# Kernel optimization log

Measured on AMD Instinct MI355X. Metric: run time of the kernel, lower is better.

Reference implementation:

```python
import jax, jax.numpy as jnp
import numpy as np

B, S, D, H = 2, 2048, 1024, 16
DK = D // H

def setup_inputs() -> dict:
    key = jax.random.key(0)
    ks = jax.random.split(key, 11)
    scale = 1.0 / np.sqrt(D)
    inp = {
        'Q': jax.random.normal(ks[0], (B, S, D), jnp.float32),
        'K': jax.random.normal(ks[1], (B, S, D), jnp.float32),
        'V': jax.random.normal(ks[2], (B, S, D), jnp.float32),
        'Wq': jax.random.normal(ks[3], (D, D), jnp.float32) * scale,
        'bq': jax.random.normal(ks[4], (D,), jnp.float32) * 0.01,
        'Wk': jax.random.normal(ks[5], (D, D), jnp.float32) * scale,
        'bk': jax.random.normal(ks[6], (D,), jnp.float32) * 0.01,
        'Wv': jax.random.normal(ks[7], (D, D), jnp.float32) * scale,
        'bv': jax.random.normal(ks[8], (D,), jnp.float32) * 0.01,
        'Wo': jax.random.normal(ks[9], (D, D), jnp.float32) * scale,
        'bo': jax.random.normal(ks[10], (D,), jnp.float32) * 0.01,
    }
    return inp

def reference(Q, K, V, Wq, bq, Wk, bk, Wv, bv, Wo, bo):
    bs = Q.shape[0]
    # projections (torch Linear: x @ W.T + b), reshape to [b, h, s, d_k]
    q = (Q @ Wq.T + bq).reshape(bs, -1, H, DK).transpose(0, 2, 1, 3)
    k = (K @ Wk.T + bk).reshape(bs, -1, H, DK).transpose(0, 2, 1, 3)
    v = (V @ Wv.T + bv).reshape(bs, -1, H, DK).transpose(0, 2, 1, 3)
    # scaled dot-product attention (no mask, dropout p=0)
    scores = jnp.einsum('bhqd,bhkd->bhqk', q, k) / np.sqrt(DK).astype(np.float32)
    attn = jax.nn.softmax(scores, axis=-1)
    ctx = jnp.einsum('bhqk,bhkd->bhqd', attn, v)
    concat = ctx.transpose(0, 2, 1, 3).reshape(bs, -1, D)
    return concat @ Wo.T + bo
```

## Files before the change

### kernel.cpp

```cpp
#include <hip/hip_runtime.h>
#include <hip/hip_bf16.h>
#include <stdint.h>

#define B_  2
#define S_  2048
#define D_  1024
#define H_  16
#define DK_ 64
#define M_  (B_ * S_)

#define QSCALE 0.18033688011112042f

typedef __attribute__((ext_vector_type(4)))  float f32x4;
typedef __attribute__((ext_vector_type(16))) float f32x16;
typedef __attribute__((ext_vector_type(8)))  short bf16x8;

__device__ __forceinline__ unsigned short f2bf(float f) {
    union { float f; unsigned u; } a; a.f = f;
    unsigned u = a.u;
    unsigned r = (u + 0x7fffu + ((u >> 16) & 1u)) >> 16;
    return (unsigned short)r;
}
__device__ __forceinline__ unsigned pk2(float lo, float hi) {
    union { float f; unsigned u; } a, b; a.f = lo; b.f = hi;
    unsigned ra = a.u + 0x7fffu + ((a.u >> 16) & 1u);
    unsigned rb = b.u + 0x7fffu + ((b.u >> 16) & 1u);
    return __builtin_amdgcn_perm(rb, ra, 0x07060302u);
}
__device__ __forceinline__ unsigned pk2f(float lo, float hi) {
    union { float f; unsigned u; } a, b; a.f = lo; b.f = hi;
    return __builtin_amdgcn_perm(b.u + 0x8000u, a.u + 0x8000u, 0x07060302u);
}

__device__ __forceinline__ void gload16(const void* g, void* l) {
    __builtin_amdgcn_global_load_lds(
        (const __attribute__((address_space(1))) void*)g,
        (__attribute__((address_space(3))) void*)l, 16, 0, 0);
}

__global__ __launch_bounds__(256) void cvt_all(
    const float* __restrict__ p0, const float* __restrict__ p1,
    const float* __restrict__ p2, const float* __restrict__ p3,
    const float* __restrict__ p4, const float* __restrict__ p5,
    const float* __restrict__ p6,
    unsigned short* __restrict__ o0, unsigned short* __restrict__ o1,
    unsigned short* __restrict__ o2, unsigned short* __restrict__ o3,
    unsigned short* __restrict__ o4, unsigned short* __restrict__ o5,
    unsigned short* __restrict__ o6) {
    const int y = blockIdx.y;
    if (y >= 3 && blockIdx.x >= 512) return;
    const float* in = (y == 0) ? p0 : (y == 1) ? p1 : (y == 2) ? p2 :
                      (y == 3) ? p3 : (y == 4) ? p4 : (y == 5) ? p5 : p6;
    unsigned short* out = (y == 0) ? o0 : (y == 1) ? o1 : (y == 2) ? o2 :
                          (y == 3) ? o3 : (y == 4) ? o4 : (y == 5) ? o5 : o6;
    const int i = blockIdx.x * 256 + threadIdx.x;
    const float4* p = (const float4*)in + (size_t)i * 2;
    float4 u = p[0], v = p[1];
    union { unsigned us[4]; bf16x8 v; } o;
    o.us[0] = pk2(u.x, u.y); o.us[1] = pk2(u.z, u.w);
    o.us[2] = pk2(v.x, v.y); o.us[3] = pk2(v.z, v.w);
    *((bf16x8*)out + i) = o.v;
}

__device__ __forceinline__ void gemm128_core(const unsigned short* __restrict__ A,
                                             const unsigned short* __restrict__ Bw,
                                             unsigned short* As, unsigned short* Bs,
                                             int brow, int bcol, f32x4 (&acc)[4][4]) {
    constexpr int K = D_;
    const int t = threadIdx.x;
    const int l = t & 63;
    const int l15 = l & 15, l4 = l >> 4;
    const int wr = (t >> 6) >> 1, wc = (t >> 6) & 1;

    const unsigned short* Ap = A + (size_t)(brow + (t >> 2)) * K + (t & 3) * 8;
    const unsigned short* Bp = Bw + (size_t)(bcol + (t >> 2)) * K + (t & 3) * 8;
    unsigned short* AsT = As + t * 8;
    unsigned short* BsT = Bs + t * 8;

    for (int k0 = 0; k0 < K; k0 += 32) {
        __syncthreads();
        gload16(Ap + k0, AsT);
        gload16(Ap + 64 * K + k0, AsT + 2048);
        gload16(Bp + k0, BsT);
        gload16(Bp + 64 * K + k0, BsT + 2048);
        __syncthreads();

        bf16x8 af[4], bfv[4];
#pragma unroll
        for (int m = 0; m < 4; m++)
            af[m] = *(const bf16x8*)(As + (wr * 64 + m * 16 + l15) * 32 + l4 * 8);
#pragma unroll
        for (int n = 0; n < 4; n++)
            bfv[n] = *(const bf16x8*)(Bs + (wc * 64 + n * 16 + l15) * 32 + l4 * 8);
#pragma unroll
        for (int m = 0; m < 4; m++)
#pragma unroll
            for (int n = 0; n < 4; n++)
                acc[m][n] = __builtin_amdgcn_mfma_f32_16x16x32_bf16(af[m], bfv[n],
                                                                    acc[m][n], 0, 0, 0);
    }
}

__global__ __launch_bounds__(256) void gemm_qkv(
    const unsigned short* __restrict__ xq, const unsigned short* __restrict__ xk,
    const unsigned short* __restrict__ xv,
    const unsigned short* __restrict__ wq, const unsigned short* __restrict__ wk,
    const unsigned short* __restrict__ wv,
    const float* __restrict__ bq, const float* __restrict__ bk,
    const float* __restrict__ bv,
    unsigned short* __restrict__ oq, unsigned short* __restrict__ ok,
    unsigned short* __restrict__ ov) {
    __shared__ unsigned short As[128 * 32];
    __shared__ unsigned short Bs[128 * 32];

    const int z = blockIdx.z;
    const unsigned short* A  = (z == 0) ? xq : (z == 1) ? xk : xv;
    const unsigned short* Bw = (z == 0) ? wq : (z == 1) ? wk : wv;
    const float* bias        = (z == 0) ? bq : (z == 1) ? bk : bv;
    unsigned short* out      = (z == 0) ? oq : (z == 1) ? ok : ov;

    const int brow = blockIdx.y * 128;
    const int bcol = blockIdx.x * 128;
    const f32x4 zf = {0.0f, 0.0f, 0.0f, 0.0f};
    f32x4 acc[4][4];
#pragma unroll
    for (int i = 0; i < 4; i++)
#pragma unroll
        for (int j = 0; j < 4; j++) acc[i][j] = zf;

    gemm128_core(A, Bw, As, Bs, brow, bcol, acc);

    const int t = threadIdx.x;
    const int l = t & 63;
    const int l15 = l & 15, l4 = l >> 4;
    const int wr = (t >> 6) >> 1, wc = (t >> 6) & 1;
    const float scale = (z == 0) ? QSCALE : 1.0f;

#pragma unroll
    for (int n = 0; n < 4; n++) {
        const int col = bcol + wc * 64 + n * 16 + l15;
        const float bia = bias[col];
        const int h = col >> 6, dk = col & 63;
#pragma unroll
        for (int m = 0; m < 4; m++) {
            const int row0 = brow + wr * 64 + m * 16 + l4 * 4;
            const int b = row0 >> 11, s0 = row0 & (S_ - 1);
            if (z != 2) {
#pragma unroll
                for (int r = 0; r < 4; r++) {
                    float v = (acc[m][n][r] + bia) * scale;
                    out[((size_t)((b * H_ + h) * S_ + (s0 + r))) * DK_ + dk] = f2bf(v);
                }
            } else {
                const int st = s0 >> 7, sl = s0 & 127;
                const int g16 = (sl >> 2) & 3;
                const int sig = ((g16 & 1) << 1) | (g16 >> 1);
                const int y = (((sl >> 4) << 5) + (sig << 3)) ^ ((dk & 7) << 4);
                uint2 o;
                o.x = pk2(acc[m][n][0] + bia, acc[m][n][1] + bia);
                o.y = pk2(acc[m][n][2] + bia, acc[m][n][3] + bia);
                *(uint2*)((char*)out +
                          ((((size_t)(b * H_ + h) * 16 + st) * 64 + dk) << 8) + y) = o;
            }
        }
    }
}

__global__ __launch_bounds__(256) void gemm_out(const unsigned short* __restrict__ A,
                                                const unsigned short* __restrict__ Bw,
                                                const float* __restrict__ bias,
                                                float* __restrict__ out) {
    __shared__ unsigned short As[128 * 32];
    __shared__ unsigned short Bs[128 * 32];

    const int brow = blockIdx.y * 128;
    const int bcol = blockIdx.x * 128;
    const f32x4 zf = {0.0f, 0.0f, 0.0f, 0.0f};
    f32x4 acc[4][4];
#pragma unroll
    for (int i = 0; i < 4; i++)
#pragma unroll
        for (int j = 0; j < 4; j++) acc[i][j] = zf;

    gemm128_core(A, Bw, As, Bs, brow, bcol, acc);

    const int t = threadIdx.x;
    const int l = t & 63;
    const int l15 = l & 15, l4 = l >> 4;
    const int wr = (t >> 6) >> 1, wc = (t >> 6) & 1;
#pragma unroll
    for (int n = 0; n < 4; n++) {
        const int col = bcol + wc * 64 + n * 16 + l15;
        const float bia = bias[col];
#pragma unroll
        for (int m = 0; m < 4; m++) {
            const int row0 = brow + wr * 64 + m * 16 + l4 * 4;
#pragma unroll
            for (int r = 0; r < 4; r++)
                out[(size_t)(row0 + r) * D_ + col] = acc[m][n][r] + bia;
        }
    }
}

__global__ __launch_bounds__(512, 4) void attn_kernel(const unsigned short* __restrict__ qh,
                                                      const unsigned short* __restrict__ kh,
                                                      const unsigned short* __restrict__ vimg,
                                                      unsigned short* __restrict__ ctx) {
    __shared__ unsigned short smem[2][16384];
    char* sm = (char*)smem;

    const int t = threadIdx.x;
    const int w = t >> 6, l = t & 63;
    const int l31 = l & 31, hi = l >> 5;
    const int hi16 = hi * 16;
    const int swz = (l31 & 7) << 4;
    const int grp = w >> 2;
    const int qs  = w & 3;

    const int bid = blockIdx.x;
    const int bh = (bid & 7) * 4 + ((bid >> 3) & 3);
    const int qt = bid >> 5;
    const int b = bh >> 4, h = bh & 15;

    const unsigned short* qg = qh + (size_t)bh * S_ * DK_;
    const unsigned short* kg = kh + (size_t)bh * S_ * DK_;

    const int q0 = qt * 128 + qs * 32;

    bf16x8 qf[4];
#pragma unroll
    for (int kc = 0; kc < 4; kc++)
        qf[kc] = *(const bf16x8*)(qg + (size_t)(q0 + l31) * DK_ + kc * 16 + hi * 8);

    const f32x16 zf16 = {0.0f};
    f32x16 acc0 = zf16, acc1 = zf16;
    float lpart = 0.0f;

    const int klr = t >> 3;
    const int kchunk = (t & 7) ^ (klr & 7);
    const unsigned short* kgp = kg + (size_t)klr * DK_ + kchunk * 8;
    auto STAGE_K = [&](int j, int buf) {
        const unsigned short* src = kgp + (size_t)j * 128 * DK_;
        char* dst = sm + buf * 32768 + t * 16;
        gload16(src, dst);
        gload16(src + 64 * DK_, dst + 8192);
    };
    const unsigned short* vgp = vimg + (size_t)bh * (16 * 8192) + t * 8;
    auto STAGE_V = [&](int j, int buf) {
        const unsigned short* src = vgp + j * 8192;
        char* dst = sm + buf * 32768 + 16384 + t * 16;
        gload16(src, dst);
        gload16(src + 4096, dst + 8192);
    };

    STAGE_K(0, 0);
    STAGE_V(0, 0);
    __syncthreads();

    constexpr int NT2 = S_ / 128;
    for (int j = 0; j < NT2; ++j) {
        const int cur = j & 1;
        if (j + 1 < NT2) {
            STAGE_K(j + 1, cur ^ 1);
            STAGE_V(j + 1, cur ^ 1);
        }

        const char* Kb = sm + cur * 32768 + grp * 8192;
        const char* Vb = sm + cur * 32768 + 16384 + grp * 128;

        f32x16 st0, st1;
        __builtin_amdgcn_s_setprio(1);
        {
            bf16x8 k0 = *(const bf16x8*)(Kb + l31 * 128 + (hi16 ^ swz));
            bf16x8 k1 = *(const bf16x8*)(Kb + (32 + l31) * 128 + (hi16 ^ swz));
            st0 = __builtin_amdgcn_mfma_f32_32x32x16_bf16(k0, qf[0], zf16, 0, 0, 0);
            st1 = __builtin_amdgcn_mfma_f32_32x32x16_bf16(k1, qf[0], zf16, 0, 0, 0);
        }
#pragma unroll
        for (int kc = 1; kc < 4; kc++) {
            bf16x8 k0 = *(const bf16x8*)(Kb + l31 * 128 + ((kc * 32 + hi16) ^ swz));
            bf16x8 k1 = *(const bf16x8*)(Kb + (32 + l31) * 128 + ((kc * 32 + hi16) ^ swz));
            st0 = __builtin_amdgcn_mfma_f32_32x32x16_bf16(k0, qf[kc], st0, 0, 0, 0);
            st1 = __builtin_amdgcn_mfma_f32_32x32x16_bf16(k1, qf[kc], st1, 0, 0, 0);
        }
        __builtin_amdgcn_s_setprio(0);

#pragma unroll
        for (int i = 0; i < 16; i++) st0[i] = exp2f(st0[i]);
#pragma unroll
        for (int i = 0; i < 16; i++) st1[i] = exp2f(st1[i]);

        float sv[8];
#pragma unroll
        for (int i = 0; i < 8; i++) sv[i] = (st0[i] + st0[i + 8]) + (st1[i] + st1[i + 8]);
#pragma unroll
        for (int s = 4; s >= 1; s >>= 1)
#pragma unroll
            for (int i = 0; i < s; i++) sv[i] += sv[i + s];
        lpart += sv[0];

        bf16x8 pf[4];
        {
            union { unsigned u[4]; bf16x8 v; } pu;
            pu.u[0] = pk2f(st0[0], st0[1]);   pu.u[1] = pk2f(st0[2], st0[3]);
            pu.u[2] = pk2f(st0[4], st0[5]);   pu.u[3] = pk2f(st0[6], st0[7]);
            pf[0] = pu.v;
            pu.u[0] = pk2f(st0[8], st0[9]);   pu.u[1] = pk2f(st0[10], st0[11]);
            pu.u[2] = pk2f(st0[12], st0[13]); pu.u[3] = pk2f(st0[14], st0[15]);
            pf[1] = pu.v;
            pu.u[0] = pk2f(st1[0], st1[1]);   pu.u[1] = pk2f(st1[2], st1[3]);
            pu.u[2] = pk2f(st1[4], st1[5]);   pu.u[3] = pk2f(st1[6], st1[7]);
            pf[2] = pu.v;
            pu.u[0] = pk2f(st1[8], st1[9]);   pu.u[1] = pk2f(st1[10], st1[11]);
            pu.u[2] = pk2f(st1[12], st1[13]); pu.u[3] = pk2f(st1[14], st1[15]);
            pf[3] = pu.v;
        }

        __builtin_amdgcn_s_setprio(1);
#pragma unroll
        for (int c = 0; c < 4; c++) {
            bf16x8 v0 = *(const bf16x8*)(Vb + l31 * 256 + ((c * 32 + hi16) ^ swz));
            bf16x8 v1 = *(const bf16x8*)(Vb + (32 + l31) * 256 + ((c * 32 + hi16) ^ swz));
            acc0 = __builtin_amdgcn_mfma_f32_32x32x16_bf16(v0, pf[c], acc0, 0, 0, 0);
            acc1 = __builtin_amdgcn_mfma_f32_32x32x16_bf16(v1, pf[c], acc1, 0, 0, 0);
        }
        __builtin_amdgcn_s_setprio(0);

        if (j + 1 < NT2) __syncthreads();
    }

    lpart += __shfl_xor(lpart, 32);
    __syncthreads();
    char* ab = sm + qs * 8192 + l31 * 256;
    const int msw = (l31 & 7) << 4;
    if (grp == 1) {
#pragma unroll
        for (int jj = 0; jj < 4; jj++) {
            f32x4 x0 = {acc0[4 * jj], acc0[4 * jj + 1], acc0[4 * jj + 2], acc0[4 * jj + 3]};
            f32x4 x1 = {acc1[4 * jj], acc1[4 * jj + 1], acc1[4 * jj + 2], acc1[4 * jj + 3]};
            *(f32x4*)(ab + ((jj * 32 + hi16) ^ msw)) = x0;
            *(f32x4*)(ab + (128 + ((jj * 32 + hi16) ^ msw))) = x1;
        }
        if (hi == 0)
            *(float*)(sm + 32768 + qs * 128 + l31 * 4) = lpart;
    }
    __syncthreads();
    if (grp == 0) {
        const float lB = *(const float*)(sm + 32768 + qs * 128 + l31 * 4);
        const float inv = 1.0f / (lpart + lB);
        unsigned short* op = ctx + ((size_t)b * S_ + (q0 + l31)) * D_ + h * 64;
#pragma unroll
        for (int jj = 0; jj < 4; jj++) {
            f32x4 b0 = *(const f32x4*)(ab + ((jj * 32 + hi16) ^ msw));
            f32x4 b1 = *(const f32x4*)(ab + (128 + ((jj * 32 + hi16) ^ msw)));
            uint2 o;
            o.x = pk2f((acc0[4 * jj + 0] + b0[0]) * inv, (acc0[4 * jj + 1] + b0[1]) * inv);
            o.y = pk2f((acc0[4 * jj + 2] + b0[2]) * inv, (acc0[4 * jj + 3] + b0[3]) * inv);
            *(uint2*)(op + jj * 8 + hi * 4) = o;
            o.x = pk2f((acc1[4 * jj + 0] + b1[0]) * inv, (acc1[4 * jj + 1] + b1[1]) * inv);
            o.y = pk2f((acc1[4 * jj + 2] + b1[2]) * inv, (acc1[4 * jj + 3] + b1[3]) * inv);
            *(uint2*)(op + 32 + jj * 8 + hi * 4) = o;
        }
    }
}

extern "C" void kernel_launch(void* const* d_in, const int* in_sizes, int n_in,
                              void* d_out, int out_size, void* d_ws, size_t ws_size,
                              hipStream_t stream) {
    const float* Q  = (const float*)d_in[0];
    const float* K  = (const float*)d_in[1];
    const float* V  = (const float*)d_in[2];
    const float* Wq = (const float*)d_in[3];
    const float* bq = (const float*)d_in[4];
    const float* Wk = (const float*)d_in[5];
    const float* bk = (const float*)d_in[6];
    const float* Wv = (const float*)d_in[7];
    const float* bv = (const float*)d_in[8];
    const float* Wo = (const float*)d_in[9];
    const float* bo = (const float*)d_in[10];

    const size_t NX = (size_t)M_ * D_;
    const size_t NW = (size_t)D_ * D_;

    unsigned short* ws = (unsigned short*)d_ws;
    unsigned short* xq  = ws; ws += NX;
    unsigned short* xk  = ws; ws += NX;
    unsigned short* xv  = ws; ws += NX;
    unsigned short* wqb = ws; ws += NW;
    unsigned short* wkb = ws; ws += NW;
    unsigned short* wvb = ws; ws += NW;
    unsigned short* wob = ws; ws += NW;
    unsigned short* qhb = ws; ws += NX;
    unsigned short* khb = ws; ws += NX;
    unsigned short* vip = ws; ws += NX;
    unsigned short* ctx = ws; ws += NX;

    cvt_all<<<dim3(2048, 7), 256, 0, stream>>>(Q, K, V, Wq, Wk, Wv, Wo,
                                               xq, xk, xv, wqb, wkb, wvb, wob);

    gemm_qkv<<<dim3(D_ / 128, M_ / 128, 3), 256, 0, stream>>>(
        xq, xk, xv, wqb, wkb, wvb, bq, bk, bv, qhb, khb, vip);

    attn_kernel<<<dim3(512), 512, 0, stream>>>(qhb, khb, vip, ctx);

    gemm_out<<<dim3(D_ / 128, M_ / 128), 256, 0, stream>>>(ctx, wob, bo, (float*)d_out);
}
```

Before: 136.8 us.

## Use fragment-ordered K/V shared-memory layout and raw exp2 in attention

Changes the K staging and the V image written by the projection GEMM so that shared memory holds data already in MFMA fragment order. Each lane can then read its operands at a fixed offset with no XOR swizzle arithmetic. Double buffering now flips precomputed offsets with XOR instead of recomputing base pointers. It also swaps exp2f for the raw hardware exp2 builtin, which drops range handling. The risk is LDS bank conflicts if the new contiguous-lane layout maps badly onto banks.

```diff
diff --git a/kernel.cpp b/kernel.cpp
--- a/kernel.cpp
+++ b/kernel.cpp
@@ -152,15 +152,16 @@
                     out[((size_t)((b * H_ + h) * S_ + (s0 + r))) * DK_ + dk] = f2bf(v);
                 }
             } else {
-                const int st = s0 >> 7, sl = s0 & 127;
-                const int g16 = (sl >> 2) & 3;
-                const int sig = ((g16 & 1) << 1) | (g16 >> 1);
-                const int y = (((sl >> 4) << 5) + (sig << 3)) ^ ((dk & 7) << 4);
+                const int st_ = s0 >> 7, sl = s0 & 127;
+                const int g = (sl >> 6) & 1, c = (sl >> 4) & 3;
+                const int j2 = (sl >> 2) & 3;
+                const int sig = ((j2 & 1) << 1) | (j2 >> 1);
                 uint2 o;
                 o.x = pk2(acc[m][n][0] + bia, acc[m][n][1] + bia);
                 o.y = pk2(acc[m][n][2] + bia, acc[m][n][3] + bia);
                 *(uint2*)((char*)out +
-                          ((((size_t)(b * H_ + h) * 16 + st) * 64 + dk) << 8) + y) = o;
+                          (((((size_t)(b * H_ + h) * 16 + st_) * 2 + g) * 4 + c) * 64 + dk) * 32 +
+                          sig * 8) = o;
             }
         }
     }
@@ -207,13 +208,12 @@
                                                       const unsigned short* __restrict__ vimg,
                                                       unsigned short* __restrict__ ctx) {
     __shared__ unsigned short smem[2][16384];
-    char* sm = (char*)smem;
+    char* smb = (char*)smem;
 
     const int t = threadIdx.x;
     const int w = t >> 6, l = t & 63;
     const int l31 = l & 31, hi = l >> 5;
     const int hi16 = hi * 16;
-    const int swz = (l31 & 7) << 4;
     const int grp = w >> 2;
     const int qs  = w & 3;
 
@@ -236,59 +236,55 @@
     f32x16 acc0 = zf16, acc1 = zf16;
     float lpart = 0.0f;
 
-    const int klr = t >> 3;
-    const int kchunk = (t & 7) ^ (klr & 7);
-    const unsigned short* kgp = kg + (size_t)klr * DK_ + kchunk * 8;
-    auto STAGE_K = [&](int j, int buf) {
-        const unsigned short* src = kgp + (size_t)j * 128 * DK_;
-        char* dst = sm + buf * 32768 + t * 16;
-        gload16(src, dst);
-        gload16(src + 64 * DK_, dst + 8192);
-    };
-    const unsigned short* vgp = vimg + (size_t)bh * (16 * 8192) + t * 8;
-    auto STAGE_V = [&](int j, int buf) {
-        const unsigned short* src = vgp + j * 8192;
-        char* dst = sm + buf * 32768 + 16384 + t * 16;
-        gload16(src, dst);
-        gload16(src + 4096, dst + 8192);
-    };
-
-    STAGE_K(0, 0);
-    STAGE_V(0, 0);
+    const int kc_ = t >> 7, key_ = (t >> 1) & 63, hi_ = t & 1;
+    const unsigned short* ksrc = kg + key_ * DK_ + kc_ * 16 + hi_ * 8;
+    const unsigned short* vsrc = vimg + (size_t)bh * (16 * 8192) + t * 8;
+
+    {
+        char* kd = smb + t * 16;
+        gload16(ksrc, kd);
+        gload16(ksrc + 4096, kd + 8192);
+        gload16(vsrc, kd + 16384);
+        gload16(vsrc + 4096, kd + 16384 + 8192);
+        ksrc += 8192; vsrc += 8192;
+    }
     __syncthreads();
 
-    constexpr int NT2 = S_ / 128;
-    for (int j = 0; j < NT2; ++j) {
-        const int cur = j & 1;
-        if (j + 1 < NT2) {
-            STAGE_K(j + 1, cur ^ 1);
-            STAGE_V(j + 1, cur ^ 1);
-        }
-
-        const char* Kb = sm + cur * 32768 + grp * 8192;
-        const char* Vb = sm + cur * 32768 + 16384 + grp * 128;
+    unsigned roff = grp * 8192 + l31 * 32 + hi16;
+    unsigned pd = 32768 + (unsigned)t * 16;
+
+    for (int j = 0; j < 16; ++j) {
+        if (j < 15) {
+            gload16(ksrc, smb + pd);
+            gload16(ksrc + 4096, smb + pd + 8192);
+            gload16(vsrc, smb + pd + 16384);
+            gload16(vsrc + 4096, smb + pd + 16384 + 8192);
+            ksrc += 8192; vsrc += 8192;
+        }
+
+        const char* Kb = smb + roff;
 
         f32x16 st0, st1;
         __builtin_amdgcn_s_setprio(1);
         {
-            bf16x8 k0 = *(const bf16x8*)(Kb + l31 * 128 + (hi16 ^ swz));
-            bf16x8 k1 = *(const bf16x8*)(Kb + (32 + l31) * 128 + (hi16 ^ swz));
+            bf16x8 k0 = *(const bf16x8*)(Kb);
+            bf16x8 k1 = *(const bf16x8*)(Kb + 1024);
             st0 = __builtin_amdgcn_mfma_f32_32x32x16_bf16(k0, qf[0], zf16, 0, 0, 0);
             st1 = __builtin_amdgcn_mfma_f32_32x32x16_bf16(k1, qf[0], zf16, 0, 0, 0);
         }
 #pragma unroll
         for (int kc = 1; kc < 4; kc++) {
-            bf16x8 k0 = *(const bf16x8*)(Kb + l31 * 128 + ((kc * 32 + hi16) ^ swz));
-            bf16x8 k1 = *(const bf16x8*)(Kb + (32 + l31) * 128 + ((kc * 32 + hi16) ^ swz));
+            bf16x8 k0 = *(const bf16x8*)(Kb + kc * 2048);
+            bf16x8 k1 = *(const bf16x8*)(Kb + kc * 2048 + 1024);
             st0 = __builtin_amdgcn_mfma_f32_32x32x16_bf16(k0, qf[kc], st0, 0, 0, 0);
             st1 = __builtin_amdgcn_mfma_f32_32x32x16_bf16(k1, qf[kc], st1, 0, 0, 0);
         }
         __builtin_amdgcn_s_setprio(0);
 
 #pragma unroll
-        for (int i = 0; i < 16; i++) st0[i] = exp2f(st0[i]);
-#pragma unroll
-        for (int i = 0; i < 16; i++) st1[i] = exp2f(st1[i]);
+        for (int i = 0; i < 16; i++) st0[i] = __builtin_amdgcn_exp2f(st0[i]);
+#pragma unroll
+        for (int i = 0; i < 16; i++) st1[i] = __builtin_amdgcn_exp2f(st1[i]);
 
         float sv[8];
 #pragma unroll
@@ -316,22 +312,25 @@
             pf[3] = pu.v;
         }
 
+        const char* Vb = smb + roff;
         __builtin_amdgcn_s_setprio(1);
 #pragma unroll
         for (int c = 0; c < 4; c++) {
-            bf16x8 v0 = *(const bf16x8*)(Vb + l31 * 256 + ((c * 32 + hi16) ^ swz));
-            bf16x8 v1 = *(const bf16x8*)(Vb + (32 + l31) * 256 + ((c * 32 + hi16) ^ swz));
+            bf16x8 v0 = *(const bf16x8*)(Vb + 16384 + c * 2048);
+            bf16x8 v1 = *(const bf16x8*)(Vb + 16384 + c * 2048 + 1024);
             acc0 = __builtin_amdgcn_mfma_f32_32x32x16_bf16(v0, pf[c], acc0, 0, 0, 0);
             acc1 = __builtin_amdgcn_mfma_f32_32x32x16_bf16(v1, pf[c], acc1, 0, 0, 0);
         }
         __builtin_amdgcn_s_setprio(0);
 
-        if (j + 1 < NT2) __syncthreads();
+        if (j < 15) __syncthreads();
+        roff ^= 32768;
+        pd ^= 32768;
     }
 
     lpart += __shfl_xor(lpart, 32);
     __syncthreads();
-    char* ab = sm + qs * 8192 + l31 * 256;
+    char* ab = smb + qs * 8192 + l31 * 256;
     const int msw = (l31 & 7) << 4;
     if (grp == 1) {
 #pragma unroll
@@ -342,11 +341,11 @@
             *(f32x4*)(ab + (128 + ((jj * 32 + hi16) ^ msw))) = x1;
         }
         if (hi == 0)
-            *(float*)(sm + 32768 + qs * 128 + l31 * 4) = lpart;
+            *(float*)(smb + 32768 + qs * 128 + l31 * 4) = lpart;
     }
     __syncthreads();
     if (grp == 0) {
-        const float lB = *(const float*)(sm + 32768 + qs * 128 + l31 * 4);
+        const float lB = *(const float*)(smb + 32768 + qs * 128 + l31 * 4);
         const float inv = 1.0f / (lpart + lB);
         unsigned short* op = ctx + ((size_t)b * S_ + (q0 + l31)) * D_ + h * 64;
 #pragma unroll
```

Measured after the change: 123.7 us. 9.6% less time.
